# Kernel tuning notes

Hardware: AMD Instinct MI355X
Metric: run time of the kernel (lower is better)

## Reference

```python
import jax, jax.numpy as jnp
import numpy as np

EPS = 1e-5

def _conv1x1(x, W, b):
    # x: [B,Ci,H,W], W: [Co,Ci]
    return jnp.einsum('oi,bihw->bohw', W, x) + b[None, :, None, None]

def _bn(x, gamma, beta, mean, var):
    # inference-mode BatchNorm2d
    s = gamma / jnp.sqrt(var + EPS)
    return x * s[None, :, None, None] + (beta - mean * s)[None, :, None, None]

def _conv3x3(x, W, b):
    y = jax.lax.conv_general_dilated(x, W, (1, 1), 'SAME',
                                     dimension_numbers=('NCHW', 'OIHW', 'NCHW'))
    return y + b[None, :, None, None]

def _sparsemax_last(S):
    # sparsemax over the last axis (TrackHSPA: max-subtract, sort, cumsum, threshold)
    S = S - jnp.max(S, axis=-1, keepdims=True)
    srt = -jnp.sort(-S, axis=-1)                 # descending sort
    csum = jnp.cumsum(srt, axis=-1) - 1.0
    N = S.shape[-1]
    ar = jnp.arange(1, N + 1, dtype=S.dtype)
    mask = ar * srt > csum
    k = jnp.sum(mask, axis=-1, keepdims=True)    # support size per row
    tau = jnp.take_along_axis(csum, k - 1, axis=-1) / k.astype(S.dtype)
    return jnp.maximum(S - tau, 0.0)

def _forward(zf, xf, Wq, bq, Ws, bs, Wg, bg, g_gamma, g_beta, g_mean, g_var,
             Wfi, bfi, fi_gamma, fi_beta, fi_mean, fi_var,
             Wm, bm, m_gamma, m_beta, m_mean, m_var, prelu_a):
    B, C, Hx, Wx = xf.shape
    # ---- Graph_Attention_Union (cross-attention) ----
    xf_t = _conv1x1(xf, Wq, bq).reshape(B, C, -1)      # [B,C,Nx]
    zf_t = _conv1x1(zf, Ws, bs).reshape(B, C, -1)      # [B,C,Nz]
    xf_g = jax.nn.relu(_bn(_conv1x1(xf, Wg, bg), g_gamma, g_beta, g_mean, g_var))
    zf_g = jax.nn.relu(_bn(_conv1x1(zf, Wg, bg), g_gamma, g_beta, g_mean, g_var))
    sim = jnp.einsum('bcn,bcm->bnm', xf_t, zf_t)       # [B,Nx,Nz]
    attn = jax.nn.softmax(sim, axis=2)
    emb = jnp.einsum('bcm,bnm->bcn', zf_g.reshape(B, C, -1), attn)
    emb = emb.reshape(B, C, Hx, Wx)
    gat = jax.nn.relu(_bn(_conv1x1(jnp.concatenate([emb, xf_g], axis=1), Wfi, bfi),
                          fi_gamma, fi_beta, fi_mean, fi_var))
    # ---- TrackHSPA (adaptive sparsemax self-attention) ----
    e = _conv3x3(gat, Wm, bm)
    e = _bn(e, m_gamma, m_beta, m_mean, m_var)
    e = jnp.where(e >= 0, e, prelu_a * e)              # PReLU (single param)
    N = Hx * Wx
    ef = e.reshape(B, -1, N)                           # [B,C',N]
    S = jnp.einsum('bdi,bdj->bij', ef, ef)             # [B,N,N]
    P = _sparsemax_last(S)
    out = jnp.einsum('bcn,bnm->bcm', gat.reshape(B, C, N), P)
    return out.reshape(B, C, Hx, Wx) + gat


def setup_inputs():
    key = jax.random.key(0)
    ks = jax.random.split(key, 8)
    B, C, Hz, Wz, Hx, Wx = 32, 256, 7, 7, 31, 31
    Cm = C // 4
    f = lambda k, shape: jax.random.normal(k, shape, jnp.float32) * 0.05
    return {
        'zf': jax.random.normal(ks[0], (B, C, Hz, Wz), jnp.float32),
        'xf': jax.random.normal(ks[1], (B, C, Hx, Wx), jnp.float32),
        'Wq': f(ks[2], (C, C)), 'bq': jnp.zeros((C,), jnp.float32),
        'Ws': f(ks[3], (C, C)), 'bs': jnp.zeros((C,), jnp.float32),
        'Wg': f(ks[4], (C, C)), 'bg': jnp.zeros((C,), jnp.float32),
        'g_gamma': jnp.ones((C,), jnp.float32), 'g_beta': jnp.zeros((C,), jnp.float32),
        'g_mean': jnp.zeros((C,), jnp.float32), 'g_var': jnp.ones((C,), jnp.float32),
        'Wfi': f(ks[5], (C, 2 * C)), 'bfi': jnp.zeros((C,), jnp.float32),
        'fi_gamma': jnp.ones((C,), jnp.float32), 'fi_beta': jnp.zeros((C,), jnp.float32),
        'fi_mean': jnp.zeros((C,), jnp.float32), 'fi_var': jnp.ones((C,), jnp.float32),
        'Wm': f(ks[6], (Cm, C, 3, 3)), 'bm': jnp.zeros((Cm,), jnp.float32),
        'm_gamma': jnp.ones((Cm,), jnp.float32), 'm_beta': jnp.zeros((Cm,), jnp.float32),
        'm_mean': jnp.zeros((Cm,), jnp.float32), 'm_var': jnp.ones((Cm,), jnp.float32),
        'prelu_a': jnp.array(0.25, jnp.float32),
    }


def reference(zf, xf, Wq, bq, Ws, bs, Wg, bg, g_gamma, g_beta, g_mean, g_var,
              Wfi, bfi, fi_gamma, fi_beta, fi_mean, fi_var,
              Wm, bm, m_gamma, m_beta, m_mean, m_var, prelu_a):
    return _forward(zf, xf, Wq, bq, Ws, bs, Wg, bg, g_gamma, g_beta, g_mean, g_var,
                    Wfi, bfi, fi_gamma, fi_beta, fi_mean, fi_var,
                    Wm, bm, m_gamma, m_beta, m_mean, m_var, prelu_a)
```

## Files before the change

kernel.cpp:

```cpp
#include <hip/hip_runtime.h>
#include <cstdint>
#include <cstddef>
#include <math.h>

typedef __attribute__((ext_vector_type(8))) short short8;
typedef __attribute__((ext_vector_type(4))) float floatx4;
typedef unsigned short ushort_t;

__device__ __forceinline__ ushort_t f2bf(float x) {
    union { float f; unsigned u; } v; v.f = x;
    unsigned r = v.u + 0x7FFF + ((v.u >> 16) & 1);
    return (ushort_t)(r >> 16);
}
__device__ __forceinline__ float bf2f(ushort_t h) {
    union { unsigned u; float f; } v; v.u = ((unsigned)h) << 16; return v.f;
}
__device__ __forceinline__ void split2(float v, ushort_t& h, ushort_t& l) {
    h = f2bf(v);
    l = f2bf(v - bf2f(h));
}

#define MFMA(a, b, c) __builtin_amdgcn_mfma_f32_16x16x32_bf16((a), (b), (c), 0, 0, 0)

__global__ void prep_all_kernel(
    const float* __restrict__ Wq, const float* __restrict__ Ws,
    const float* __restrict__ Wg, const float* __restrict__ Wfi,
    const float* __restrict__ Wm,
    const float* bq, const float* bs,
    const float* bg, const float* gg, const float* gb, const float* gm, const float* gv,
    const float* bfi, const float* fg, const float* fb, const float* fm, const float* fv,
    const float* bm, const float* mg, const float* mb, const float* mm, const float* mv,
    ushort_t* Wq_h, ushort_t* Wq_l, ushort_t* Ws_h, ushort_t* Ws_l,
    ushort_t* Wg_h, ushort_t* Wg_l, ushort_t* Wfi_h, ushort_t* Wfi_l,
    ushort_t* wm_h, ushort_t* wm_l, float* scsh)
{
    int bid = blockIdx.x, t = threadIdx.x;
    if (bid < 256) {
        int i = bid * 256 + t; ushort_t h, l; split2(Wq[i], h, l); Wq_h[i] = h; Wq_l[i] = l;
    } else if (bid < 512) {
        int i = (bid - 256) * 256 + t; ushort_t h, l; split2(Ws[i], h, l); Ws_h[i] = h; Ws_l[i] = l;
    } else if (bid < 768) {
        int i = (bid - 512) * 256 + t; ushort_t h, l; split2(Wg[i], h, l); Wg_h[i] = h; Wg_l[i] = l;
    } else if (bid < 1280) {
        int i = (bid - 768) * 256 + t; ushort_t h, l; split2(Wfi[i], h, l); Wfi_h[i] = h; Wfi_l[i] = l;
    } else if (bid < 1856) {
        int i = (bid - 1280) * 256 + t;
        int c = i & 255, m = (i >> 8) & 63, tap = i >> 14;
        ushort_t h, l; split2(Wm[((size_t)m * 256 + c) * 9 + tap], h, l);
        wm_h[i] = h; wm_l[i] = l;
    } else {
        if (t < 256) {
            scsh[t] = 1.f;        scsh[256 + t] = bq[t];
            scsh[512 + t] = 1.f;  scsh[768 + t] = bs[t];
            float s = gg[t] * rsqrtf(gv[t] + 1e-5f);
            scsh[1024 + t] = s;   scsh[1280 + t] = gb[t] + s * (bg[t] - gm[t]);
            float s2 = fg[t] * rsqrtf(fv[t] + 1e-5f);
            scsh[1536 + t] = s2;  scsh[1792 + t] = fb[t] + s2 * (bfi[t] - fm[t]);
            if (t < 64) {
                float s3 = mg[t] * rsqrtf(mv[t] + 1e-5f);
                scsh[2048 + t] = s3; scsh[2112 + t] = mb[t] + s3 * (bm[t] - mm[t]);
            }
        }
    }
}

__global__ void halo_zero_kernel(ushort_t* __restrict__ gxh, ushort_t* __restrict__ gxl) {
    int i = blockIdx.x * 256 + threadIdx.x;
    int b = i >> 7, k = i & 127;
    int r;
    if (k < 33) r = k;
    else if (k < 66) r = 32 * 33 + (k - 33);
    else { int k2 = k - 66; r = ((k2 >> 1) + 1) * 33 + ((k2 & 1) ? 32 : 0); }
    uint4* ph = (uint4*)(gxh + ((size_t)b * 1089 + r) * 256);
    uint4* pl = (uint4*)(gxl + ((size_t)b * 1089 + r) * 256);
    uint4 z = make_uint4(0, 0, 0, 0);
#pragma unroll
    for (int s = 0; s < 32; s++) { ph[s] = z; pl[s] = z; }
}

__global__ __launch_bounds__(256) void transpose_in_kernel(
    const float* __restrict__ in, ushort_t* __restrict__ oh, ushort_t* __restrict__ ol,
    int Nsrc, int Npad)
{
    int b = blockIdx.z;
    const float* ib = in + (size_t)b * 256 * Nsrc;
    ushort_t* obh = oh + (size_t)b * Npad * 256;
    ushort_t* obl = ol + (size_t)b * Npad * 256;
    __shared__ float tile[32][33];
    int n0 = blockIdx.x * 32, c0 = blockIdx.y * 32;
    int tx = threadIdx.x & 31, ty = threadIdx.x >> 5;
#pragma unroll
    for (int r = 0; r < 4; r++) {
        int c = c0 + ty + r * 8, n = n0 + tx;
        tile[ty + r * 8][tx] = (n < Nsrc) ? ib[(size_t)c * Nsrc + n] : 0.f;
    }
    __syncthreads();
#pragma unroll
    for (int r = 0; r < 4; r++) {
        int n = n0 + ty + r * 8, c = c0 + tx;
        if (n < Nsrc) {
            ushort_t h, l; split2(tile[tx][ty + r * 8], h, l);
            obh[(size_t)n * 256 + c] = h;
            obl[(size_t)n * 256 + c] = l;
        }
    }
}

__global__ __launch_bounds__(256, 2) void dualconv_mfma_kernel(
    const ushort_t* __restrict__ Xh, const ushort_t* __restrict__ Xl,
    const ushort_t* __restrict__ W1h, const ushort_t* __restrict__ W1l,
    const ushort_t* __restrict__ W2h, const ushort_t* __restrict__ W2l,
    const float* __restrict__ sc1, const float* __restrict__ sh1,
    const float* __restrict__ sc2, const float* __restrict__ sh2,
    int relu1, int relu2,
    ushort_t* __restrict__ O1h, ushort_t* __restrict__ O1l,
    ushort_t* __restrict__ O2h, ushort_t* __restrict__ O2l,
    ushort_t* __restrict__ O2ch, ushort_t* __restrict__ O2cl, int cpitch,
    int K, int Nvalid, int NpadIn, int NpadOut)
{
    int b = blockIdx.x;
    int half = blockIdx.y & 1;
    int n0 = (blockIdx.y >> 1) * 64;
    const ushort_t* Xbh = Xh + (size_t)b * NpadIn * K;
    const ushort_t* Xbl = Xl + (size_t)b * NpadIn * K;
    int tid = threadIdx.x, w = tid >> 6, l = tid & 63, lc = l & 15, q = l >> 4;
    int m0 = w * 64;

    const ushort_t* Wh = half ? W2h : W1h;
    const ushort_t* Wl = half ? W2l : W1l;
    const float* sc = half ? sc2 : sc1;
    const float* sh = half ? sh2 : sh1;
    int relu = half ? relu2 : relu1;
    ushort_t* Obh = (half ? O2h : O1h) + (size_t)b * NpadOut * 256;
    ushort_t* Obl = (half ? O2l : O1l) + (size_t)b * NpadOut * 256;

    int nrow[4];
#pragma unroll
    for (int jt = 0; jt < 4; jt++) {
        int nr = n0 + jt * 16 + lc;
        nrow[jt] = (nr < NpadIn) ? nr : (NpadIn - 1);
    }

    floatx4 acc[4][4];
#pragma unroll
    for (int i = 0; i < 4; i++)
#pragma unroll
        for (int j = 0; j < 4; j++) acc[i][j] = (floatx4){0.f, 0.f, 0.f, 0.f};

#define DC_LOADA(K0, AH, AL) do { \
    _Pragma("unroll") \
    for (int mt_ = 0; mt_ < 4; mt_++) { \
        size_t off_ = (size_t)(m0 + mt_ * 16 + lc) * K + (K0) + q * 8; \
        AH[mt_] = *(const short8*)(Wh + off_); \
        AL[mt_] = *(const short8*)(Wl + off_); \
    } \
} while (0)
#define DC_LOADB(K0, BH, BL) do { \
    _Pragma("unroll") \
    for (int jt_ = 0; jt_ < 4; jt_++) { \
        size_t off_ = (size_t)nrow[jt_] * K + (K0) + q * 8; \
        BH[jt_] = *(const short8*)(Xbh + off_); \
        BL[jt_] = *(const short8*)(Xbl + off_); \
    } \
} while (0)
#define DC_MFMA(AH, AL, BH, BL) do { \
    _Pragma("unroll") \
    for (int mt_ = 0; mt_ < 4; mt_++) \
    _Pragma("unroll") \
    for (int jt_ = 0; jt_ < 4; jt_++) { \
        acc[mt_][jt_] = MFMA(AH[mt_], BH[jt_], acc[mt_][jt_]); \
        acc[mt_][jt_] = MFMA(AH[mt_], BL[jt_], acc[mt_][jt_]); \
        acc[mt_][jt_] = MFMA(AL[mt_], BH[jt_], acc[mt_][jt_]); \
    } \
} while (0)

    short8 ah0[4], al0[4], bh0[4], bl0[4];
    short8 ah1[4], al1[4], bh1[4], bl1[4];
    DC_LOADA(0, ah0, al0);
    DC_LOADB(0, bh0, bl0);
    for (int k0 = 0; k0 < K; k0 += 64) {
        DC_LOADA(k0 + 32, ah1, al1);
        DC_LOADB(k0 + 32, bh1, bl1);
        DC_MFMA(ah0, al0, bh0, bl0);
        if (k0 + 64 < K) {
            DC_LOADA(k0 + 64, ah0, al0);
            DC_LOADB(k0 + 64, bh0, bl0);
        }
        DC_MFMA(ah1, al1, bh1, bl1);
    }
#undef DC_LOADA
#undef DC_LOADB
#undef DC_MFMA

#pragma unroll
    for (int mt = 0; mt < 4; mt++) {
        int mb = m0 + mt * 16 + q * 4;
        float s0 = sc[mb], s1 = sc[mb + 1], s2 = sc[mb + 2], s3 = sc[mb + 3];
        float h0 = sh[mb], h1 = sh[mb + 1], h2 = sh[mb + 2], h3 = sh[mb + 3];
#pragma unroll
        for (int jt = 0; jt < 4; jt++) {
            int n = n0 + jt * 16 + lc;
            if (n >= Nvalid) continue;
            float v0 = acc[mt][jt][0] * s0 + h0;
            float v1 = acc[mt][jt][1] * s1 + h1;
            float v2 = acc[mt][jt][2] * s2 + h2;
            float v3 = acc[mt][jt][3] * s3 + h3;
            if (relu) { v0 = fmaxf(v0, 0.f); v1 = fmaxf(v1, 0.f); v2 = fmaxf(v2, 0.f); v3 = fmaxf(v3, 0.f); }
            ushort_t e0, f0, e1, f1, e2, f2, e3, f3;
            split2(v0, e0, f0); split2(v1, e1, f1); split2(v2, e2, f2); split2(v3, e3, f3);
            *(ushort4*)(Obh + (size_t)n * 256 + mb) = make_ushort4(e0, e1, e2, e3);
            *(ushort4*)(Obl + (size_t)n * 256 + mb) = make_ushort4(f0, f1, f2, f3);
            if (half && O2ch) {
                O2ch[((size_t)b * 256 + mb + 0) * cpitch + n] = e0;
                O2ch[((size_t)b * 256 + mb + 1) * cpitch + n] = e1;
                O2ch[((size_t)b * 256 + mb + 2) * cpitch + n] = e2;
                O2ch[((size_t)b * 256 + mb + 3) * cpitch + n] = e3;
                O2cl[((size_t)b * 256 + mb + 0) * cpitch + n] = f0;
                O2cl[((size_t)b * 256 + mb + 1) * cpitch + n] = f1;
                O2cl[((size_t)b * 256 + mb + 2) * cpitch + n] = f2;
                O2cl[((size_t)b * 256 + mb + 3) * cpitch + n] = f3;
            }
        }
    }
}

__global__ __launch_bounds__(256) void attn_mfma_kernel(
    const ushort_t* __restrict__ xth, const ushort_t* __restrict__ xtl,
    const ushort_t* __restrict__ zth, const ushort_t* __restrict__ ztl,
    const ushort_t* __restrict__ zgh, const ushort_t* __restrict__ zgl,
    ushort_t* __restrict__ eh, ushort_t* __restrict__ el)
{
    __shared__ float S[64][68];
    __shared__ ushort_t awh[64][72], awl[64][72];
    __shared__ float T[4][16][20];
    int b = blockIdx.x, n0 = blockIdx.y * 64;
    int tid = threadIdx.x, w = tid >> 6, l = tid & 63, lc = l & 15, q = l >> 4;
    const ushort_t* xhb = xth + (size_t)b * 992 * 256;
    const ushort_t* xlb = xtl + (size_t)b * 992 * 256;
    const ushort_t* zhb = zth + (size_t)b * 64 * 256;
    const ushort_t* zlb = ztl + (size_t)b * 64 * 256;
    const ushort_t* ghb = zgh + (size_t)b * 256 * 64;
    const ushort_t* glb = zgl + (size_t)b * 256 * 64;

    int rowg = n0 + w * 16 + lc;
#pragma unroll
    for (int ct = 0; ct < 4; ct++) {
        floatx4 acc = (floatx4){0.f, 0.f, 0.f, 0.f};
        for (int k0 = 0; k0 < 256; k0 += 32) {
            short8 ah = *(const short8*)(xhb + (size_t)rowg * 256 + k0 + q * 8);
            short8 al = *(const short8*)(xlb + (size_t)rowg * 256 + k0 + q * 8);
            short8 bh = *(const short8*)(zhb + (size_t)(ct * 16 + lc) * 256 + k0 + q * 8);
            short8 bl = *(const short8*)(zlb + (size_t)(ct * 16 + lc) * 256 + k0 + q * 8);
            acc = MFMA(ah, bh, acc);
            acc = MFMA(ah, bl, acc);
            acc = MFMA(al, bh, acc);
        }
#pragma unroll
        for (int r = 0; r < 4; r++) S[w * 16 + q * 4 + r][ct * 16 + lc] = acc[r];
    }
    __syncthreads();
    if (tid < 64) {
        float mx = -INFINITY;
        for (int m = 0; m < 49; m++) mx = fmaxf(mx, S[tid][m]);
        float sum = 0.f;
        for (int m = 0; m < 49; m++) { float e = __expf(S[tid][m] - mx); S[tid][m] = e; sum += e; }
        float inv = 1.f / sum;
        for (int m = 0; m < 64; m++) {
            float vv = (m < 49) ? S[tid][m] * inv : 0.f;
            ushort_t hh, ll; split2(vv, hh, ll);
            awh[tid][m] = hh; awl[tid][m] = ll;
        }
    }
    __syncthreads();
    int nw = l >> 2, cg = l & 3;
#pragma unroll
    for (int ct = 0; ct < 16; ct++) {
        floatx4 acc = (floatx4){0.f, 0.f, 0.f, 0.f};
#pragma unroll
        for (int k0 = 0; k0 < 64; k0 += 32) {
            short8 ah = *(const short8*)(&awh[w * 16 + lc][k0 + q * 8]);
            short8 al = *(const short8*)(&awl[w * 16 + lc][k0 + q * 8]);
            short8 bh = *(const short8*)(ghb + (size_t)(ct * 16 + lc) * 64 + k0 + q * 8);
            short8 bl = *(const short8*)(glb + (size_t)(ct * 16 + lc) * 64 + k0 + q * 8);
            acc = MFMA(ah, bh, acc);
            acc = MFMA(ah, bl, acc);
            acc = MFMA(al, bh, acc);
        }
#pragma unroll
        for (int r = 0; r < 4; r++) T[w][q * 4 + r][lc] = acc[r];
        float4 vv = *(const float4*)&T[w][nw][cg * 4];
        int n = n0 + w * 16 + nw;
        if (n < 961) {
            ushort_t h0, l0, h1, l1, h2, l2_, h3, l3;
            split2(vv.x, h0, l0); split2(vv.y, h1, l1);
            split2(vv.z, h2, l2_); split2(vv.w, h3, l3);
            size_t off = ((size_t)b * 992 + n) * 256 + ct * 16 + cg * 4;
            *(ushort4*)(eh + off) = make_ushort4(h0, h1, h2, h3);
            *(ushort4*)(el + off) = make_ushort4(l0, l1, l2_, l3);
        }
    }
}

__global__ __launch_bounds__(256) void fi_mfma_kernel(
    const ushort_t* __restrict__ Eh, const ushort_t* __restrict__ El,
    const ushort_t* __restrict__ Gh, const ushort_t* __restrict__ Gl,
    const ushort_t* __restrict__ Wh, const ushort_t* __restrict__ Wl,
    const float* __restrict__ sc, const float* __restrict__ sh,
    ushort_t* __restrict__ gxh, ushort_t* __restrict__ gxl,
    ushort_t* __restrict__ gat_nf)
{
    int b = blockIdx.x;
    const ushort_t* Ebh = Eh + (size_t)b * 992 * 256;
    const ushort_t* Ebl = El + (size_t)b * 992 * 256;
    const ushort_t* Gbh = Gh + (size_t)b * 992 * 256;
    const ushort_t* Gbl = Gl + (size_t)b * 992 * 256;
    ushort_t* gxhb = gxh + (size_t)b * 1089 * 256;
    ushort_t* gxlb = gxl + (size_t)b * 1089 * 256;
    ushort_t* gn = gat_nf + (size_t)b * 256 * 992;
    int tid = threadIdx.x, w = tid >> 6, l = tid & 63, lc = l & 15, q = l >> 4;
    int m0 = w * 64, nb0 = blockIdx.y * 32;

    floatx4 acc[4][2];
#pragma unroll
    for (int i = 0; i < 4; i++)
#pragma unroll
        for (int j = 0; j < 2; j++) acc[i][j] = (floatx4){0.f, 0.f, 0.f, 0.f};

#define FI_LOADB(K0, BH, BL) do { \
    const ushort_t* sh__ = ((K0) < 256) ? Ebh : Gbh; \
    const ushort_t* sl__ = ((K0) < 256) ? Ebl : Gbl; \
    int kk_ = ((K0) < 256) ? (K0) : (K0) - 256; \
    _Pragma("unroll") \
    for (int jt_ = 0; jt_ < 2; jt_++) { \
        size_t off_ = (size_t)(nb0 + jt_ * 16 + lc) * 256 + kk_ + q * 8; \
        BH[jt_] = *(const short8*)(sh__ + off_); \
        BL[jt_] = *(const short8*)(sl__ + off_); \
    } \
} while (0)
#define FI_MFMA(BH, BL) do { \
    _Pragma("unroll") \
    for (int mt_ = 0; mt_ < 4; mt_++) \
    _Pragma("unroll") \
    for (int jt_ = 0; jt_ < 2; jt_++) { \
        acc[mt_][jt_] = MFMA(ah[mt_], BH[jt_], acc[mt_][jt_]); \
        acc[mt_][jt_] = MFMA(ah[mt_], BL[jt_], acc[mt_][jt_]); \
        acc[mt_][jt_] = MFMA(al[mt_], BH[jt_], acc[mt_][jt_]); \
    } \
} while (0)

    short8 bh0[2], bl0[2], bh1[2], bl1[2];
    FI_LOADB(0, bh0, bl0);
    for (int k0 = 0; k0 < 512; k0 += 64) {
        short8 ah[4], al[4];
#pragma unroll
        for (int mt = 0; mt < 4; mt++) {
            size_t off = (size_t)(m0 + mt * 16 + lc) * 512 + k0 + q * 8;
            ah[mt] = *(const short8*)(Wh + off);
            al[mt] = *(const short8*)(Wl + off);
        }
        FI_LOADB(k0 + 32, bh1, bl1);
        FI_MFMA(bh0, bl0);
#pragma unroll
        for (int mt = 0; mt < 4; mt++) {
            size_t off = (size_t)(m0 + mt * 16 + lc) * 512 + k0 + 32 + q * 8;
            ah[mt] = *(const short8*)(Wh + off);
            al[mt] = *(const short8*)(Wl + off);
        }
        if (k0 + 64 < 512) FI_LOADB(k0 + 64, bh0, bl0);
        FI_MFMA(bh1, bl1);
    }
#undef FI_LOADB
#undef FI_MFMA

#pragma unroll
    for (int mt = 0; mt < 4; mt++) {
        int mb = m0 + mt * 16 + q * 4;
        float s0 = sc[mb], s1 = sc[mb + 1], s2 = sc[mb + 2], s3 = sc[mb + 3];
        float h0 = sh[mb], h1 = sh[mb + 1], h2 = sh[mb + 2], h3 = sh[mb + 3];
#pragma unroll
        for (int jt = 0; jt < 2; jt++) {
            int n = nb0 + jt * 16 + lc;
            if (n >= 961) continue;
            float v0 = fmaxf(acc[mt][jt][0] * s0 + h0, 0.f);
            float v1 = fmaxf(acc[mt][jt][1] * s1 + h1, 0.f);
            float v2 = fmaxf(acc[mt][jt][2] * s2 + h2, 0.f);
            float v3 = fmaxf(acc[mt][jt][3] * s3 + h3, 0.f);
            ushort_t a0, b0, a1, b1, a2, b2, a3, b3;
            split2(v0, a0, b0); split2(v1, a1, b1); split2(v2, a2, b2); split2(v3, a3, b3);
            int hh = n / 31, ww2 = n - hh * 31;
            int row = (hh + 1) * 33 + (ww2 + 1);
            *(ushort4*)(gxhb + (size_t)row * 256 + mb) = make_ushort4(a0, a1, a2, a3);
            *(ushort4*)(gxlb + (size_t)row * 256 + mb) = make_ushort4(b0, b1, b2, b3);
            gn[(size_t)(mb + 0) * 992 + n] = a0;
            gn[(size_t)(mb + 1) * 992 + n] = a1;
            gn[(size_t)(mb + 2) * 992 + n] = a2;
            gn[(size_t)(mb + 3) * 992 + n] = a3;
        }
    }
}

__global__ __launch_bounds__(256, 2) void conv3x3_mfma_kernel(
    const ushort_t* __restrict__ gxh, const ushort_t* __restrict__ gxl,
    const ushort_t* __restrict__ wmh, const ushort_t* __restrict__ wml,
    const float* __restrict__ sc, const float* __restrict__ sh,
    const float* __restrict__ prelu_a,
    ushort_t* __restrict__ eh, ushort_t* __restrict__ el)
{
    __shared__ float Sp[4][2048];
    int b = blockIdx.x;
    const ushort_t* gxhb = gxh + (size_t)b * 1089 * 256;
    const ushort_t* gxlb = gxl + (size_t)b * 1089 * 256;
    ushort_t* ebh = eh + (size_t)b * 1024 * 64;
    ushort_t* ebl = el + (size_t)b * 1024 * 64;
    int tid = threadIdx.x, w = tid >> 6, l = tid & 63, lc = l & 15, q = l >> 4;
    int j0 = blockIdx.y * 64;

    int base[4];
#pragma unroll
    for (int jt = 0; jt < 4; jt++) {
        int j = j0 + jt * 16 + lc; if (j > 960) j = 960;
        int hh = j / 31, ww2 = j - hh * 31;
        base[jt] = (hh + 1) * 33 + (ww2 + 1);
    }

    floatx4 acc[4][4];
#pragma unroll
    for (int i = 0; i < 4; i++)
#pragma unroll
        for (int j = 0; j < 4; j++) acc[i][j] = (floatx4){0.f, 0.f, 0.f, 0.f};

#define C3_LOAD(SL, AH, AL, BH, BL) do { \
    int sl_ = (SL); \
    int tap_ = (sl_ >= 9) ? sl_ - 9 : sl_; \
    int k0_ = (w * 2 + ((sl_ >= 9) ? 1 : 0)) * 32; \
    int doff_ = (tap_ / 3 - 1) * 33 + (tap_ % 3 - 1); \
    const ushort_t* wth_ = wmh + tap_ * 16384; \
    const ushort_t* wtl_ = wml + tap_ * 16384; \
    _Pragma("unroll") \
    for (int mt_ = 0; mt_ < 4; mt_++) { \
        size_t off_ = (size_t)(mt_ * 16 + lc) * 256 + k0_ + q * 8; \
        AH[mt_] = *(const short8*)(wth_ + off_); \
        AL[mt_] = *(const short8*)(wtl_ + off_); \
    } \
    _Pragma("unroll") \
    for (int jt_ = 0; jt_ < 4; jt_++) { \
        size_t off_ = (size_t)(base[jt_] + doff_) * 256 + k0_ + q * 8; \
        BH[jt_] = *(const short8*)(gxhb + off_); \
        BL[jt_] = *(const short8*)(gxlb + off_); \
    } \
} while (0)
#define C3_MFMA(AH, AL, BH, BL) do { \
    _Pragma("unroll") \
    for (int mt_ = 0; mt_ < 4; mt_++) \
    _Pragma("unroll") \
    for (int jt_ = 0; jt_ < 4; jt_++) { \
        acc[mt_][jt_] = MFMA(AH[mt_], BH[jt_], acc[mt_][jt_]); \
        acc[mt_][jt_] = MFMA(AH[mt_], BL[jt_], acc[mt_][jt_]); \
        acc[mt_][jt_] = MFMA(AL[mt_], BH[jt_], acc[mt_][jt_]); \
    } \
} while (0)

    short8 A0h[4], A0l[4], B0h[4], B0l[4];
    short8 A1h[4], A1l[4], B1h[4], B1l[4];
    C3_LOAD(0, A0h, A0l, B0h, B0l);
#pragma unroll
    for (int it = 0; it < 9; it++) {
        C3_LOAD(it * 2 + 1, A1h, A1l, B1h, B1l);
        C3_MFMA(A0h, A0l, B0h, B0l);
        if (it < 8) C3_LOAD(it * 2 + 2, A0h, A0l, B0h, B0l);
        C3_MFMA(A1h, A1l, B1h, B1l);
    }
#undef C3_LOAD
#undef C3_MFMA

    float pa = prelu_a[0];
#pragma unroll
    for (int ph = 0; ph < 2; ph++) {
        __syncthreads();
#pragma unroll
        for (int mt = 0; mt < 4; mt++)
#pragma unroll
            for (int jt = 0; jt < 2; jt++)
#pragma unroll
                for (int r = 0; r < 4; r++)
                    Sp[w][(mt * 16 + q * 4 + r) * 32 + jt * 16 + lc] = acc[mt][ph * 2 + jt][r];
        __syncthreads();
#pragma unroll
        for (int gi = 0; gi < 2; gi++) {
            int g = tid + gi * 256;
            int j = g & 31, mg = g >> 5;
            int m = mg * 4;
            int jj = j0 + ph * 32 + j;
            if (jj >= 961) continue;
            float v[4];
#pragma unroll
            for (int i = 0; i < 4; i++) {
                int idx = (m + i) * 32 + j;
                v[i] = Sp[0][idx] + Sp[1][idx] + Sp[2][idx] + Sp[3][idx];
                v[i] = v[i] * sc[m + i] + sh[m + i];
                v[i] = v[i] >= 0.f ? v[i] : pa * v[i];
            }
            ushort_t a0, b0, a1, b1, a2, b2, a3, b3;
            split2(v[0], a0, b0); split2(v[1], a1, b1);
            split2(v[2], a2, b2); split2(v[3], a3, b3);
            *(ushort4*)(ebh + (size_t)jj * 64 + m) = make_ushort4(a0, a1, a2, a3);
            *(ushort4*)(ebl + (size_t)jj * 64 + m) = make_ushort4(b0, b1, b2, b3);
        }
    }
}

__global__ __launch_bounds__(512) void hspa_mfma_kernel(
    const ushort_t* __restrict__ eh, const ushort_t* __restrict__ el,
    ushort_t* __restrict__ PT)
{
    const int PITCH = 978;
    __shared__ float S[16 * 978];
    int b = blockIdx.x, nb = blockIdx.y;
    const ushort_t* ebh = eh + (size_t)b * 1024 * 64;
    const ushort_t* ebl = el + (size_t)b * 1024 * 64;
    ushort_t* Pb = PT + (size_t)b * 1024 * 992;
    int tid = threadIdx.x, w = tid >> 6, l = tid & 63, lc = l & 15, q = l >> 4;
    int n0 = nb * 16;

    short8 a0h = *(const short8*)(ebh + (size_t)(n0 + lc) * 64 + q * 8);
    short8 a0l = *(const short8*)(ebl + (size_t)(n0 + lc) * 64 + q * 8);
    short8 a1h = *(const short8*)(ebh + (size_t)(n0 + lc) * 64 + 32 + q * 8);
    short8 a1l = *(const short8*)(ebl + (size_t)(n0 + lc) * 64 + 32 + q * 8);

    for (int jt = w; jt < 61; jt += 8) {
        int j = jt * 16 + lc;
        short8 b0h = *(const short8*)(ebh + (size_t)j * 64 + q * 8);
        short8 b0l = *(const short8*)(ebl + (size_t)j * 64 + q * 8);
        short8 b1h = *(const short8*)(ebh + (size_t)j * 64 + 32 + q * 8);
        short8 b1l = *(const short8*)(ebl + (size_t)j * 64 + 32 + q * 8);
        floatx4 acc = (floatx4){0.f, 0.f, 0.f, 0.f};
        acc = MFMA(a0h, b0h, acc);
        acc = MFMA(a0h, b0l, acc);
        acc = MFMA(a0l, b0h, acc);
        acc = MFMA(a1h, b1h, acc);
        acc = MFMA(a1h, b1l, acc);
        acc = MFMA(a1l, b1h, acc);
#pragma unroll
        for (int r = 0; r < 4; r++) S[(q * 4 + r) * PITCH + j] = acc[r];
    }
    __syncthreads();

    int r0 = w * 2, r1 = w * 2 + 1;
    float sv0[16], sv1[16];
    float mx0 = -INFINITY, mx1 = -INFINITY;
#pragma unroll
    for (int t = 0; t < 16; t++) {
        int j = l + t * 64;
        float s0 = (j < 961) ? S[r0 * PITCH + j] : -INFINITY;
        float s1 = (j < 961) ? S[r1 * PITCH + j] : -INFINITY;
        sv0[t] = s0; sv1[t] = s1;
        mx0 = fmaxf(mx0, s0); mx1 = fmaxf(mx1, s1);
    }
    for (int off = 32; off; off >>= 1) {
        mx0 = fmaxf(mx0, __shfl_xor(mx0, off));
        mx1 = fmaxf(mx1, __shfl_xor(mx1, off));
    }
#pragma unroll
    for (int t = 0; t < 16; t++) { sv0[t] -= mx0; sv1[t] -= mx1; }

    float tau0 = -1.f, tau1 = -1.f;
    for (int it = 0; it < 16; it++) {
        float s0 = 0.f, c0 = 0.f, s1 = 0.f, c1 = 0.f;
#pragma unroll
        for (int t = 0; t < 16; t++) {
            if (sv0[t] > tau0) { s0 += sv0[t]; c0 += 1.f; }
            if (sv1[t] > tau1) { s1 += sv1[t]; c1 += 1.f; }
        }
        for (int off = 32; off; off >>= 1) {
            s0 += __shfl_xor(s0, off); c0 += __shfl_xor(c0, off);
            s1 += __shfl_xor(s1, off); c1 += __shfl_xor(c1, off);
        }
        float nt0 = (s0 - 1.f) / c0;
        float nt1 = (s1 - 1.f) / c1;
        bool conv = (nt0 == tau0) && (nt1 == tau1);
        tau0 = nt0; tau1 = nt1;
        if (conv) break;
    }
#pragma unroll
    for (int t = 0; t < 16; t++) {
        int j = l + t * 64;
        if (j < 976) {
            S[r0 * PITCH + j] = (j < 961) ? fmaxf(sv0[t] - tau0, 0.f) : 0.f;
            S[r1 * PITCH + j] = (j < 961) ? fmaxf(sv1[t] - tau1, 0.f) : 0.f;
        }
    }
    __syncthreads();

    for (int j = tid; j < 976; j += 512) {
        union { ushort_t u[8]; uint4 v; } p0, p1;
#pragma unroll
        for (int r = 0; r < 8; r++)  p0.u[r] = f2bf(S[r * PITCH + j]);
#pragma unroll
        for (int r = 0; r < 8; r++)  p1.u[r] = f2bf(S[(8 + r) * PITCH + j]);
        ushort_t* dst = Pb + (size_t)j * 992 + n0;
        *(uint4*)(dst) = p0.v;
        *(uint4*)(dst + 8) = p1.v;
    }
}

__global__ __launch_bounds__(256, 2) void out_mfma_kernel(
    const ushort_t* __restrict__ gat_nf, const ushort_t* __restrict__ PT,
    float* __restrict__ out)
{
    int b = blockIdx.x, jb = blockIdx.y;
    const ushort_t* gb = gat_nf + (size_t)b * 256 * 992;
    const ushort_t* Pb = PT + (size_t)b * 1024 * 992;
    float* ob = out + (size_t)b * 256 * 961;
    int tid = threadIdx.x, w = tid >> 6, l = tid & 63, lc = l & 15, q = l >> 4;
    int m0 = w * 64, j0 = jb * 64;

    floatx4 acc[4][4];
#pragma unroll
    for (int i = 0; i < 4; i++)
#pragma unroll
        for (int j = 0; j < 4; j++) acc[i][j] = (floatx4){0.f, 0.f, 0.f, 0.f};

#define OUT_LOAD(K0, AA, BB) do { \
    _Pragma("unroll") \
    for (int mt_ = 0; mt_ < 4; mt_++) \
        AA[mt_] = *(const short8*)(gb + (size_t)(m0 + mt_ * 16 + lc) * 992 + (K0) + q * 8); \
    _Pragma("unroll") \
    for (int jt_ = 0; jt_ < 4; jt_++) \
        BB[jt_] = *(const short8*)(Pb + (size_t)(j0 + jt_ * 16 + lc) * 992 + (K0) + q * 8); \
} while (0)
#define OUT_MFMA(AA, BB) do { \
    _Pragma("unroll") \
    for (int mt_ = 0; mt_ < 4; mt_++) \
    _Pragma("unroll") \
    for (int jt_ = 0; jt_ < 4; jt_++) \
        acc[mt_][jt_] = MFMA(AA[mt_], BB[jt_], acc[mt_][jt_]); \
} while (0)

    short8 a0[4], b0[4], a1[4], b1[4];
    OUT_LOAD(0, a0, b0);
    for (int k0 = 0; k0 < 960; k0 += 64) {
        OUT_LOAD(k0 + 32, a1, b1);
        OUT_MFMA(a0, b0);
        OUT_LOAD(k0 + 64, a0, b0);
        OUT_MFMA(a1, b1);
    }
    OUT_MFMA(a0, b0);
#undef OUT_LOAD
#undef OUT_MFMA

#pragma unroll
    for (int mt = 0; mt < 4; mt++) {
        int mb = m0 + mt * 16 + q * 4;
#pragma unroll
        for (int jt = 0; jt < 4; jt++) {
            int j = j0 + jt * 16 + lc;
            if (j >= 961) continue;
#pragma unroll
            for (int r = 0; r < 4; r++) {
                float g = bf2f(gb[(size_t)(mb + r) * 992 + j]);
                ob[(size_t)(mb + r) * 961 + j] = acc[mt][jt][r] + g;
            }
        }
    }
}

extern "C" void kernel_launch(void* const* d_in, const int* in_sizes, int n_in,
                              void* d_out, int out_size, void* d_ws, size_t ws_size,
                              hipStream_t stream)
{
    const float* zf      = (const float*)d_in[0];
    const float* xf      = (const float*)d_in[1];
    const float* Wq      = (const float*)d_in[2];
    const float* bq      = (const float*)d_in[3];
    const float* Ws      = (const float*)d_in[4];
    const float* bs      = (const float*)d_in[5];
    const float* Wg      = (const float*)d_in[6];
    const float* bg      = (const float*)d_in[7];
    const float* g_gamma = (const float*)d_in[8];
    const float* g_beta  = (const float*)d_in[9];
    const float* g_mean  = (const float*)d_in[10];
    const float* g_var   = (const float*)d_in[11];
    const float* Wfi     = (const float*)d_in[12];
    const float* bfi     = (const float*)d_in[13];
    const float* fi_gamma= (const float*)d_in[14];
    const float* fi_beta = (const float*)d_in[15];
    const float* fi_mean = (const float*)d_in[16];
    const float* fi_var  = (const float*)d_in[17];
    const float* Wm      = (const float*)d_in[18];
    const float* bm      = (const float*)d_in[19];
    const float* m_gamma = (const float*)d_in[20];
    const float* m_beta  = (const float*)d_in[21];
    const float* m_mean  = (const float*)d_in[22];
    const float* m_var   = (const float*)d_in[23];
    const float* prelu_a = (const float*)d_in[24];
    float* out = (float*)d_out;

    ushort_t* ws = (ushort_t*)d_ws;
    ushort_t* Wq_h  = ws + 0;         ushort_t* Wq_l  = ws + 65536;
    ushort_t* Ws_h  = ws + 131072;    ushort_t* Ws_l  = ws + 196608;
    ushort_t* Wg_h  = ws + 262144;    ushort_t* Wg_l  = ws + 327680;
    ushort_t* Wfi_h = ws + 393216;    ushort_t* Wfi_l = ws + 524288;
    ushort_t* wm_h  = ws + 655360;    ushort_t* wm_l  = ws + 802816;
    ushort_t* XT_h    = ws + 950272;
    ushort_t* XT_l    = ws + 9076736;
    ushort_t* xf_tT_h = ws + 17203200;
    ushort_t* xf_tT_l = ws + 25329664;
    ushort_t* zf_tT_h = ws + 33456128;
    ushort_t* zf_tT_l = ws + 33980416;
    ushort_t* zf_gT_h = ws + 34504704;
    ushort_t* zf_gT_l = ws + 35028992;
    ushort_t* gxT_h   = ws + 17203200;
    ushort_t* gxT_l   = ws + 26124288;
    ushort_t* xf_gT_h = ws + 35553280;
    ushort_t* xf_gT_l = ws + 43679744;
    ushort_t* gat_nf  = ws + 51806208;
    ushort_t* eT_h    = ws + 59932672;
    ushort_t* eT_l    = ws + 62029824;
    ushort_t* PT      = ws + 64126976;
    ushort_t* zfT_h   = ws + 96632832;
    ushort_t* zfT_l   = ws + 97157120;
    float* scsh       = (float*)(ws + 97681408);
    ushort_t* zgC_h   = ws + 97685760;
    ushort_t* zgC_l   = ws + 98210048;
    ushort_t* embT_h = XT_h;
    ushort_t* embT_l = XT_l;

    const float* sc_q  = scsh + 0,    *sh_q  = scsh + 256;
    const float* sc_s  = scsh + 512,  *sh_s  = scsh + 768;
    const float* sc_g  = scsh + 1024, *sh_g  = scsh + 1280;
    const float* sc_fi = scsh + 1536, *sh_fi = scsh + 1792;
    const float* sc_m  = scsh + 2048, *sh_m  = scsh + 2112;

    prep_all_kernel<<<1857, 256, 0, stream>>>(
        Wq, Ws, Wg, Wfi, Wm,
        bq, bs, bg, g_gamma, g_beta, g_mean, g_var,
        bfi, fi_gamma, fi_beta, fi_mean, fi_var,
        bm, m_gamma, m_beta, m_mean, m_var,
        Wq_h, Wq_l, Ws_h, Ws_l, Wg_h, Wg_l, Wfi_h, Wfi_l, wm_h, wm_l, scsh);

    transpose_in_kernel<<<dim3(31, 8, 32), 256, 0, stream>>>(xf, XT_h, XT_l, 961, 992);
    transpose_in_kernel<<<dim3(2, 8, 32), 256, 0, stream>>>(zf, zfT_h, zfT_l, 49, 64);

    dualconv_mfma_kernel<<<dim3(32, 32), 256, 0, stream>>>(
        XT_h, XT_l, Wq_h, Wq_l, Wg_h, Wg_l,
        sc_q, sh_q, sc_g, sh_g, 0, 1,
        xf_tT_h, xf_tT_l, xf_gT_h, xf_gT_l,
        nullptr, nullptr, 0, 256, 961, 992, 992);
    dualconv_mfma_kernel<<<dim3(32, 2), 256, 0, stream>>>(
        zfT_h, zfT_l, Ws_h, Ws_l, Wg_h, Wg_l,
        sc_s, sh_s, sc_g, sh_g, 0, 1,
        zf_tT_h, zf_tT_l, zf_gT_h, zf_gT_l,
        zgC_h, zgC_l, 64, 256, 49, 64, 64);

    attn_mfma_kernel<<<dim3(32, 16), 256, 0, stream>>>(
        xf_tT_h, xf_tT_l, zf_tT_h, zf_tT_l, zgC_h, zgC_l, embT_h, embT_l);

    halo_zero_kernel<<<16, 256, 0, stream>>>(gxT_h, gxT_l);

    fi_mfma_kernel<<<dim3(32, 31), 256, 0, stream>>>(
        embT_h, embT_l, xf_gT_h, xf_gT_l, Wfi_h, Wfi_l, sc_fi, sh_fi,
        gxT_h, gxT_l, gat_nf);

    conv3x3_mfma_kernel<<<dim3(32, 16), 256, 0, stream>>>(
        gxT_h, gxT_l, wm_h, wm_l, sc_m, sh_m, prelu_a, eT_h, eT_l);

    hspa_mfma_kernel<<<dim3(32, 61), 512, 0, stream>>>(eT_h, eT_l, PT);

    out_mfma_kernel<<<dim3(32, 16), 256, 0, stream>>>(gat_nf, PT, out);
}
```

Measured before the change: 608.2 us.

## Stage activation tiles in LDS via direct global-to-LDS loads, share across both convs

```diff
diff --git a/kernel.cpp b/kernel.cpp
--- a/kernel.cpp
+++ b/kernel.cpp
@@ -21,6 +21,12 @@
 }
 
 #define MFMA(a, b, c) __builtin_amdgcn_mfma_f32_16x16x32_bf16((a), (b), (c), 0, 0, 0)
+
+__device__ __forceinline__ void gload_lds16(const void* g, void* l) {
+    __builtin_amdgcn_global_load_lds(
+        (const __attribute__((address_space(1))) unsigned*)g,
+        (__attribute__((address_space(3))) unsigned*)l, 16, 0, 0);
+}
 
 __global__ void prep_all_kernel(
     const float* __restrict__ Wq, const float* __restrict__ Ws,
@@ -118,34 +124,26 @@
     ushort_t* __restrict__ O2ch, ushort_t* __restrict__ O2cl, int cpitch,
     int K, int Nvalid, int NpadIn, int NpadOut)
 {
+    __shared__ ushort_t Bs[32768];
     int b = blockIdx.x;
-    int half = blockIdx.y & 1;
-    int n0 = (blockIdx.y >> 1) * 64;
+    int n0 = blockIdx.y * 64;
     const ushort_t* Xbh = Xh + (size_t)b * NpadIn * K;
     const ushort_t* Xbl = Xl + (size_t)b * NpadIn * K;
     int tid = threadIdx.x, w = tid >> 6, l = tid & 63, lc = l & 15, q = l >> 4;
     int m0 = w * 64;
 
-    const ushort_t* Wh = half ? W2h : W1h;
-    const ushort_t* Wl = half ? W2l : W1l;
-    const float* sc = half ? sc2 : sc1;
-    const float* sh = half ? sh2 : sh1;
-    int relu = half ? relu2 : relu1;
-    ushort_t* Obh = (half ? O2h : O1h) + (size_t)b * NpadOut * 256;
-    ushort_t* Obl = (half ? O2l : O1l) + (size_t)b * NpadOut * 256;
-
-    int nrow[4];
-#pragma unroll
-    for (int jt = 0; jt < 4; jt++) {
-        int nr = n0 + jt * 16 + lc;
-        nrow[jt] = (nr < NpadIn) ? nr : (NpadIn - 1);
-    }
-
-    floatx4 acc[4][4];
-#pragma unroll
-    for (int i = 0; i < 4; i++)
-#pragma unroll
-        for (int j = 0; j < 4; j++) acc[i][j] = (floatx4){0.f, 0.f, 0.f, 0.f};
+#pragma unroll
+    for (int r = 0; r < 16; r++) {
+        int d = r * 4096 + w * 1024 + l * 16;
+        int dr = d & 32767;
+        int row = dr >> 9;
+        int inrow = (dr & 511) ^ ((row & 7) << 4);
+        int srow = n0 + row; if (srow > NpadIn - 1) srow = NpadIn - 1;
+        const ushort_t* src = ((d >> 15) ? Xbl : Xbh) + (size_t)srow * K + (inrow >> 1);
+        char* dst = (char*)Bs + (r * 4096 + w * 1024);
+        gload_lds16(src, dst);
+    }
+    __syncthreads();
 
 #define DC_LOADA(K0, AH, AL) do { \
     _Pragma("unroll") \
@@ -155,12 +153,13 @@
         AL[mt_] = *(const short8*)(Wl + off_); \
     } \
 } while (0)
-#define DC_LOADB(K0, BH, BL) do { \
+#define DC_LDSB(K0, BH, BL) do { \
     _Pragma("unroll") \
     for (int jt_ = 0; jt_ < 4; jt_++) { \
-        size_t off_ = (size_t)nrow[jt_] * K + (K0) + q * 8; \
-        BH[jt_] = *(const short8*)(Xbh + off_); \
-        BL[jt_] = *(const short8*)(Xbl + off_); \
+        int row_ = jt_ * 16 + lc; \
+        int koff_ = (((K0) + q * 8) * 2) ^ ((row_ & 7) << 4); \
+        BH[jt_] = *(const short8*)((const char*)Bs + row_ * 512 + koff_); \
+        BL[jt_] = *(const short8*)((const char*)Bs + 32768 + row_ * 512 + koff_); \
     } \
 } while (0)
 #define DC_MFMA(AH, AL, BH, BL) do { \
@@ -174,54 +173,66 @@
     } \
 } while (0)
 
-    short8 ah0[4], al0[4], bh0[4], bl0[4];
-    short8 ah1[4], al1[4], bh1[4], bl1[4];
-    DC_LOADA(0, ah0, al0);
-    DC_LOADB(0, bh0, bl0);
-    for (int k0 = 0; k0 < K; k0 += 64) {
-        DC_LOADA(k0 + 32, ah1, al1);
-        DC_LOADB(k0 + 32, bh1, bl1);
-        DC_MFMA(ah0, al0, bh0, bl0);
-        if (k0 + 64 < K) {
-            DC_LOADA(k0 + 64, ah0, al0);
-            DC_LOADB(k0 + 64, bh0, bl0);
-        }
-        DC_MFMA(ah1, al1, bh1, bl1);
+    for (int half = 0; half < 2; half++) {
+        const ushort_t* Wh = half ? W2h : W1h;
+        const ushort_t* Wl = half ? W2l : W1l;
+        const float* sc = half ? sc2 : sc1;
+        const float* sh = half ? sh2 : sh1;
+        int relu = half ? relu2 : relu1;
+        ushort_t* Obh = (half ? O2h : O1h) + (size_t)b * NpadOut * 256;
+        ushort_t* Obl = (half ? O2l : O1l) + (size_t)b * NpadOut * 256;
+
+        floatx4 acc[4][4];
+#pragma unroll
+        for (int i = 0; i < 4; i++)
+#pragma unroll
+            for (int j = 0; j < 4; j++) acc[i][j] = (floatx4){0.f, 0.f, 0.f, 0.f};
+
+        short8 ah0[4], al0[4], ah1[4], al1[4], bh[4], bl[4];
+        DC_LOADA(0, ah0, al0);
+        for (int k0 = 0; k0 < K; k0 += 64) {
+            DC_LOADA(k0 + 32, ah1, al1);
+            DC_LDSB(k0, bh, bl);
+            DC_MFMA(ah0, al0, bh, bl);
+            if (k0 + 64 < K) DC_LOADA(k0 + 64, ah0, al0);
+            DC_LDSB(k0 + 32, bh, bl);
+            DC_MFMA(ah1, al1, bh, bl);
+        }
+
+#pragma unroll
+        for (int mt = 0; mt < 4; mt++) {
+            int mb = m0 + mt * 16 + q * 4;
+            float s0 = sc[mb], s1 = sc[mb + 1], s2 = sc[mb + 2], s3 = sc[mb + 3];
+            float h0 = sh[mb], h1 = sh[mb + 1], h2 = sh[mb + 2], h3 = sh[mb + 3];
+#pragma unroll
+            for (int jt = 0; jt < 4; jt++) {
+                int n = n0 + jt * 16 + lc;
+                if (n >= Nvalid) continue;
+                float v0 = acc[mt][jt][0] * s0 + h0;
+                float v1 = acc[mt][jt][1] * s1 + h1;
+                float v2 = acc[mt][jt][2] * s2 + h2;
+                float v3 = acc[mt][jt][3] * s3 + h3;
+                if (relu) { v0 = fmaxf(v0, 0.f); v1 = fmaxf(v1, 0.f); v2 = fmaxf(v2, 0.f); v3 = fmaxf(v3, 0.f); }
+                ushort_t e0, f0, e1, f1, e2, f2, e3, f3;
+                split2(v0, e0, f0); split2(v1, e1, f1); split2(v2, e2, f2); split2(v3, e3, f3);
+                *(ushort4*)(Obh + (size_t)n * 256 + mb) = make_ushort4(e0, e1, e2, e3);
+                *(ushort4*)(Obl + (size_t)n * 256 + mb) = make_ushort4(f0, f1, f2, f3);
+                if (half && O2ch) {
+                    O2ch[((size_t)b * 256 + mb + 0) * cpitch + n] = e0;
+                    O2ch[((size_t)b * 256 + mb + 1) * cpitch + n] = e1;
+                    O2ch[((size_t)b * 256 + mb + 2) * cpitch + n] = e2;
+                    O2ch[((size_t)b * 256 + mb + 3) * cpitch + n] = e3;
+                    O2cl[((size_t)b * 256 + mb + 0) * cpitch + n] = f0;
+                    O2cl[((size_t)b * 256 + mb + 1) * cpitch + n] = f1;
+                    O2cl[((size_t)b * 256 + mb + 2) * cpitch + n] = f2;
+                    O2cl[((size_t)b * 256 + mb + 3) * cpitch + n] = f3;
+                }
+            }
+        }
     }
 #undef DC_LOADA
-#undef DC_LOADB
+#undef DC_LDSB
 #undef DC_MFMA
-
-#pragma unroll
-    for (int mt = 0; mt < 4; mt++) {
-        int mb = m0 + mt * 16 + q * 4;
-        float s0 = sc[mb], s1 = sc[mb + 1], s2 = sc[mb + 2], s3 = sc[mb + 3];
-        float h0 = sh[mb], h1 = sh[mb + 1], h2 = sh[mb + 2], h3 = sh[mb + 3];
-#pragma unroll
-        for (int jt = 0; jt < 4; jt++) {
-            int n = n0 + jt * 16 + lc;
-            if (n >= Nvalid) continue;
-            float v0 = acc[mt][jt][0] * s0 + h0;
-            float v1 = acc[mt][jt][1] * s1 + h1;
-            float v2 = acc[mt][jt][2] * s2 + h2;
-            float v3 = acc[mt][jt][3] * s3 + h3;
-            if (relu) { v0 = fmaxf(v0, 0.f); v1 = fmaxf(v1, 0.f); v2 = fmaxf(v2, 0.f); v3 = fmaxf(v3, 0.f); }
-            ushort_t e0, f0, e1, f1, e2, f2, e3, f3;
-            split2(v0, e0, f0); split2(v1, e1, f1); split2(v2, e2, f2); split2(v3, e3, f3);
-            *(ushort4*)(Obh + (size_t)n * 256 + mb) = make_ushort4(e0, e1, e2, e3);
-            *(ushort4*)(Obl + (size_t)n * 256 + mb) = make_ushort4(f0, f1, f2, f3);
-            if (half && O2ch) {
-                O2ch[((size_t)b * 256 + mb + 0) * cpitch + n] = e0;
-                O2ch[((size_t)b * 256 + mb + 1) * cpitch + n] = e1;
-                O2ch[((size_t)b * 256 + mb + 2) * cpitch + n] = e2;
-                O2ch[((size_t)b * 256 + mb + 3) * cpitch + n] = e3;
-                O2cl[((size_t)b * 256 + mb + 0) * cpitch + n] = f0;
-                O2cl[((size_t)b * 256 + mb + 1) * cpitch + n] = f1;
-                O2cl[((size_t)b * 256 + mb + 2) * cpitch + n] = f2;
-                O2cl[((size_t)b * 256 + mb + 3) * cpitch + n] = f3;
-            }
-        }
-    }
 }
 
 __global__ __launch_bounds__(256) void attn_mfma_kernel(
@@ -301,7 +312,7 @@
     }
 }
 
-__global__ __launch_bounds__(256) void fi_mfma_kernel(
+__global__ __launch_bounds__(256, 2) void fi_mfma_kernel(
     const ushort_t* __restrict__ Eh, const ushort_t* __restrict__ El,
     const ushort_t* __restrict__ Gh, const ushort_t* __restrict__ Gl,
     const ushort_t* __restrict__ Wh, const ushort_t* __restrict__ Wl,
@@ -309,6 +320,7 @@
     ushort_t* __restrict__ gxh, ushort_t* __restrict__ gxl,
     ushort_t* __restrict__ gat_nf)
 {
+    __shared__ ushort_t Bs[32768];
     int b = blockIdx.x;
     const ushort_t* Ebh = Eh + (size_t)b * 992 * 256;
     const ushort_t* Ebl = El + (size_t)b * 992 * 256;
@@ -320,56 +332,71 @@
     int tid = threadIdx.x, w = tid >> 6, l = tid & 63, lc = l & 15, q = l >> 4;
     int m0 = w * 64, nb0 = blockIdx.y * 32;
 
+#pragma unroll
+    for (int r = 0; r < 16; r++) {
+        int d = r * 4096 + w * 1024 + l * 16;
+        int seg = d >> 14;
+        int dr = d & 16383;
+        int row = dr >> 9;
+        int inrow = (dr & 511) ^ ((row & 7) << 4);
+        int srow = nb0 + row; if (srow > 991) srow = 991;
+        const ushort_t* base = (seg == 0) ? Ebh : (seg == 1) ? Ebl : (seg == 2) ? Gbh : Gbl;
+        const ushort_t* src = base + (size_t)srow * 256 + (inrow >> 1);
+        char* dst = (char*)Bs + (r * 4096 + w * 1024);
+        gload_lds16(src, dst);
+    }
+    __syncthreads();
+
     floatx4 acc[4][2];
 #pragma unroll
     for (int i = 0; i < 4; i++)
 #pragma unroll
         for (int j = 0; j < 2; j++) acc[i][j] = (floatx4){0.f, 0.f, 0.f, 0.f};
 
-#define FI_LOADB(K0, BH, BL) do { \
-    const ushort_t* sh__ = ((K0) < 256) ? Ebh : Gbh; \
-    const ushort_t* sl__ = ((K0) < 256) ? Ebl : Gbl; \
-    int kk_ = ((K0) < 256) ? (K0) : (K0) - 256; \
+#define FI_LOADA(K0, AH, AL) do { \
+    _Pragma("unroll") \
+    for (int mt_ = 0; mt_ < 4; mt_++) { \
+        size_t off_ = (size_t)(m0 + mt_ * 16 + lc) * 512 + (K0) + q * 8; \
+        AH[mt_] = *(const short8*)(Wh + off_); \
+        AL[mt_] = *(const short8*)(Wl + off_); \
+    } \
+} while (0)
+#define FI_LDSB(K0, BH, BL) do { \
+    int segb_ = ((K0) < 256) ? 0 : 32768; \
+    int kk_ = (K0) & 255; \
     _Pragma("unroll") \
     for (int jt_ = 0; jt_ < 2; jt_++) { \
-        size_t off_ = (size_t)(nb0 + jt_ * 16 + lc) * 256 + kk_ + q * 8; \
-        BH[jt_] = *(const short8*)(sh__ + off_); \
-        BL[jt_] = *(const short8*)(sl__ + off_); \
-    } \
-} while (0)
-#define FI_MFMA(BH, BL) do { \
+        int row_ = jt_ * 16 + lc; \
+        int koff_ = ((kk_ + q * 8) * 2) ^ ((row_ & 7) << 4); \
+        BH[jt_] = *(const short8*)((const char*)Bs + segb_ + row_ * 512 + koff_); \
+        BL[jt_] = *(const short8*)((const char*)Bs + segb_ + 16384 + row_ * 512 + koff_); \
+    } \
+} while (0)
+#define FI_MFMA(AH, AL, BH, BL) do { \
     _Pragma("unroll") \
     for (int mt_ = 0; mt_ < 4; mt_++) \
     _Pragma("unroll") \
     for (int jt_ = 0; jt_ < 2; jt_++) { \
-        acc[mt_][jt_] = MFMA(ah[mt_], BH[jt_], acc[mt_][jt_]); \
-        acc[mt_][jt_] = MFMA(ah[mt_], BL[jt_], acc[mt_][jt_]); \
-        acc[mt_][jt_] = MFMA(al[mt_], BH[jt_], acc[mt_][jt_]); \
-    } \
-} while (0)
-
-    short8 bh0[2], bl0[2], bh1[2], bl1[2];
-    FI_LOADB(0, bh0, bl0);
-    for (int k0 = 0; k0 < 512; k0 += 64) {
-        short8 ah[4], al[4];
-#pragma unroll
-        for (int mt = 0; mt < 4; mt++) {
-            size_t off = (size_t)(m0 + mt * 16 + lc) * 512 + k0 + q * 8;
-            ah[mt] = *(const short8*)(Wh + off);
-            al[mt] = *(const short8*)(Wl + off);
-        }
-        FI_LOADB(k0 + 32, bh1, bl1);
-        FI_MFMA(bh0, bl0);
-#pragma unroll
-        for (int mt = 0; mt < 4; mt++) {
-            size_t off = (size_t)(m0 + mt * 16 + lc) * 512 + k0 + 32 + q * 8;
-            ah[mt] = *(const short8*)(Wh + off);
-            al[mt] = *(const short8*)(Wl + off);
-        }
-        if (k0 + 64 < 512) FI_LOADB(k0 + 64, bh0, bl0);
-        FI_MFMA(bh1, bl1);
-    }
-#undef FI_LOADB
+        acc[mt_][jt_] = MFMA(AH[mt_], BH[jt_], acc[mt_][jt_]); \
+        acc[mt_][jt_] = MFMA(AH[mt_], BL[jt_], acc[mt_][jt_]); \
+        acc[mt_][jt_] = MFMA(AL[mt_], BH[jt_], acc[mt_][jt_]); \
+    } \
+} while (0)
+
+    {
+        short8 ah0[4], al0[4], ah1[4], al1[4], bh[2], bl[2];
+        FI_LOADA(0, ah0, al0);
+        for (int k0 = 0; k0 < 512; k0 += 64) {
+            FI_LOADA(k0 + 32, ah1, al1);
+            FI_LDSB(k0, bh, bl);
+            FI_MFMA(ah0, al0, bh, bl);
+            if (k0 + 64 < 512) FI_LOADA(k0 + 64, ah0, al0);
+            FI_LDSB(k0 + 32, bh, bl);
+            FI_MFMA(ah1, al1, bh, bl);
+        }
+    }
+#undef FI_LOADA
+#undef FI_LDSB
 #undef FI_MFMA
 
 #pragma unroll
@@ -741,12 +768,12 @@
     transpose_in_kernel<<<dim3(31, 8, 32), 256, 0, stream>>>(xf, XT_h, XT_l, 961, 992);
     transpose_in_kernel<<<dim3(2, 8, 32), 256, 0, stream>>>(zf, zfT_h, zfT_l, 49, 64);
 
-    dualconv_mfma_kernel<<<dim3(32, 32), 256, 0, stream>>>(
+    dualconv_mfma_kernel<<<dim3(32, 16), 256, 0, stream>>>(
         XT_h, XT_l, Wq_h, Wq_l, Wg_h, Wg_l,
         sc_q, sh_q, sc_g, sh_g, 0, 1,
         xf_tT_h, xf_tT_l, xf_gT_h, xf_gT_l,
         nullptr, nullptr, 0, 256, 961, 992, 992);
-    dualconv_mfma_kernel<<<dim3(32, 2), 256, 0, stream>>>(
+    dualconv_mfma_kernel<<<dim3(32, 1), 256, 0, stream>>>(
         zfT_h, zfT_l, Ws_h, Ws_l, Wg_h, Wg_l,
         sc_s, sh_s, sc_g, sh_g, 0, 1,
         zf_tT_h, zf_tT_l, zf_gT_h, zf_gT_l,
```

Result: faster. 580.5 us (-4.6%).
